# Kernel optimization log

Hardware: AMD Instinct MI355X
Metric: run time of the kernel (lower is better)

## Reference

```python
import math
import jax, jax.numpy as jnp
import numpy as np

B, S, DK, DV = 8, 2048, 512, 512

def setup_inputs() -> dict:
    key = jax.random.key(0)
    kq, kk, kv, km = jax.random.split(key, 4)
    Q = jax.random.normal(kq, (B, S, DK), dtype=jnp.float32)
    K = jax.random.normal(kk, (B, S, DK), dtype=jnp.float32)
    V = jax.random.normal(kv, (B, S, DV), dtype=jnp.float32)
    # key-padding mask, True = masked out; broadcasts over query dim
    mask_out = jax.random.randint(km, (B, 1, S), 0, 2).astype(jnp.bool_)
    return {"Q": Q, "K": K, "V": V, "mask_out": mask_out}

def reference(Q, K, V, mask_out):
    scale = math.sqrt(Q.shape[-1])
    # [B, S, S] scores
    scores = jnp.einsum('bqd,bkd->bqk', Q, K) / scale
    scores = jnp.where(mask_out, -jnp.inf, scores)
    attn = jax.nn.softmax(scores, axis=-1)
    # dropout is identity in eval mode (reference baseline)
    return jnp.einsum('bqk,bkv->bqv', attn, V)
```

## Files before the change

kernel.cpp:

```cpp
#include <hip/hip_runtime.h>
#include <stdint.h>
#include <stddef.h>

#define B_ 8
#define S_ 2048
#define D_ 512
#define QT 64
#define KTL 32
#define NIT (S_ / KTL)

typedef __attribute__((ext_vector_type(8))) short short8;
typedef __attribute__((ext_vector_type(4))) float f32x4;

#define OFF_K0  0
#define OFF_K1  32768
#define OFF_ST  65536
#define OFF_P   73728
#define OFF_A   77824
#define OFF_L   78080
#define OFF_M   78336
#define LDS_BYTES 78592

__device__ __forceinline__ void gl_lds16(const void* g, void* l) {
  __builtin_amdgcn_global_load_lds(
      (const __attribute__((address_space(1))) uint32_t*)g,
      (__attribute__((address_space(3))) uint32_t*)l, 16, 0, 0);
}

__device__ __forceinline__ void bar_lgkm() {
  __asm__ __volatile__("" ::: "memory");
  __builtin_amdgcn_s_waitcnt(0xC07F);
  __builtin_amdgcn_s_barrier();
  __asm__ __volatile__("" ::: "memory");
}
__device__ __forceinline__ void bar_vm0() {
  __asm__ __volatile__("" ::: "memory");
  __builtin_amdgcn_s_waitcnt(0x0070);
  __builtin_amdgcn_s_barrier();
  __asm__ __volatile__("" ::: "memory");
}

template<int CTRL>
__device__ __forceinline__ float dpp_mov(float x) {
  return __builtin_bit_cast(float,
      __builtin_amdgcn_update_dpp(0, __builtin_bit_cast(int, x),
                                  CTRL, 0xF, 0xF, true));
}
__device__ __forceinline__ float red8_max(float x) {
  x = fmaxf(x, dpp_mov<0xB1>(x));
  x = fmaxf(x, dpp_mov<0x4E>(x));
  x = fmaxf(x, dpp_mov<0x141>(x));
  return x;
}
__device__ __forceinline__ float red8_sum(float x) {
  x += dpp_mov<0xB1>(x);
  x += dpp_mov<0x4E>(x);
  x += dpp_mov<0x141>(x);
  return x;
}

__device__ __forceinline__ uint32_t f2bf(float f) {
  union { float f; uint32_t u; } x; x.f = f;
  uint32_t r = x.u + 0x7FFFu + ((x.u >> 16) & 1u);
  return r >> 16;
}

__device__ __forceinline__ bool sniff_fp32(const void* p) {
  const uint32_t* w = (const uint32_t*)p;
  bool ok = true;
  #pragma unroll 1
  for (int i = 0; i < 64; ++i) {
    uint32_t e = (w[i] >> 23) & 0xFFu;
    if (!(e == 0u || (e >= 64u && e <= 192u))) ok = false;
  }
  return ok;
}

__device__ __forceinline__ short8 cvt8(const void* src, bool fp32) {
  short8 d;
  if (fp32) {
    const float* s = (const float*)src;
    f32x4 a = *(const f32x4*)s, c = *(const f32x4*)(s + 4);
    #pragma unroll
    for (int j = 0; j < 4; ++j) { d[j] = (short)f2bf(a[j]); d[4 + j] = (short)f2bf(c[j]); }
  } else {
    d = *(const short8*)src;
  }
  return d;
}

__global__ void prep_kernel(const void* __restrict__ K, const void* __restrict__ V,
                            uint16_t* __restrict__ kbf, uint16_t* __restrict__ vt) {
  __shared__ uint32_t vtile[64 * 32];
  bool fp32 = sniff_fp32(K);
  int kt = blockIdx.x, dt = blockIdx.y, b = blockIdx.z;
  int t  = threadIdx.x;
  {
    size_t off = (size_t)b * S_ * D_ + (size_t)(kt * 64 + (t >> 3)) * D_ + dt * 64 + (t & 7) * 8;
    const void* src = fp32 ? (const void*)((const float*)K + off)
                           : (const void*)((const uint16_t*)K + off);
    *(short8*)(kbf + off) = cvt8(src, fp32);
  }
  {
    int key = t >> 3;
    int c0  = (t & 7) * 4;
    size_t off = (size_t)b * S_ * D_ + (size_t)(kt * 64 + key) * D_ + dt * 64 + (t & 7) * 8;
    const void* src = fp32 ? (const void*)((const float*)V + off)
                           : (const void*)((const uint16_t*)V + off);
    short8 d = cvt8(src, fp32);
    const uint32_t* dw = (const uint32_t*)&d;
    #pragma unroll
    for (int i = 0; i < 4; ++i)
      vtile[key * 32 + ((c0 + i + key) & 31)] = dw[i];
  }
  __syncthreads();
  {
    int dvl = t >> 3;
    int kg  = t & 7;
    short8 o;
    #pragma unroll
    for (int j = 0; j < 8; ++j) {
      int key = kg * 8 + j;
      uint32_t wv = vtile[key * 32 + (((dvl >> 1) + key) & 31)];
      o[j] = (short)((dvl & 1) ? (wv >> 16) : (wv & 0xFFFFu));
    }
    *(short8*)(vt + ((size_t)b * D_ + dt * 64 + dvl) * S_ + kt * 64 + kg * 8) = o;
  }
}

__device__ __forceinline__ void stage_K(char* buf, const uint16_t* kg, int w, int lane, int kt) {
  #pragma unroll
  for (int p = 0; p < 4; ++p) {
    int n = p * 8 + w;
    int g = (lane & ~7) | ((lane ^ n) & 7);
    gl_lds16(kg + ((size_t)(kt * KTL + n)) * D_ + g * 8, buf + n * 1024);
  }
}
__device__ __forceinline__ void stage_K_slow(char* buf, const void* kg, bool fp32,
                                             int w, int lane, int kt) {
  #pragma unroll
  for (int p = 0; p < 4; ++p) {
    int n = p * 8 + w;
    size_t off = ((size_t)(kt * KTL + n)) * D_ + lane * 8;
    const void* src = fp32 ? (const void*)((const float*)kg + off)
                           : (const void*)((const uint16_t*)kg + off);
    short8 d = cvt8(src, fp32);
    int s = (lane & ~7) | ((lane ^ n) & 7);
    *(short8*)(buf + n * 1024 + s * 16) = d;
  }
}
__device__ __forceinline__ void stage_V_slow(char* smem, const void* vg, bool fp32,
                                             int w, int lane, int kt) {
  #pragma unroll
  for (int p = 0; p < 4; ++p) {
    int n = p * 8 + w;
    size_t off = ((size_t)(kt * KTL + n)) * D_ + lane * 8;
    const void* src = fp32 ? (const void*)((const float*)vg + off)
                           : (const void*)((const uint16_t*)vg + off);
    short8 d = cvt8(src, fp32);
    *(short8*)(smem + OFF_K1 + n * 1024 + lane * 16) = d;
  }
}

template<bool FAST>
__global__ __launch_bounds__(512, 2)
void attn_kernel(const void* __restrict__ Q, const void* __restrict__ K,
                 const void* __restrict__ V, const void* __restrict__ mask,
                 const uint16_t* __restrict__ kbf, const uint16_t* __restrict__ vtbf,
                 void* __restrict__ out) {
  extern __shared__ char smem[];
  const int tid  = threadIdx.x;
  const int lane = tid & 63;
  const int w    = tid >> 6;
  const int m15  = lane & 15;
  const int kq   = lane >> 4;

  const bool fp32 = sniff_fp32(Q);

  const int b     = blockIdx.x;
  const int qbase = blockIdx.y * QT;
  const int qt_w  = w >> 1;
  const int kh    = w & 1;

  const uint16_t* kgf  = FAST ? (kbf + (size_t)b * S_ * D_) : nullptr;
  const uint16_t* vtg  = FAST ? (vtbf + (size_t)b * D_ * S_) : nullptr;
  const void* kgs = fp32 ? (const void*)((const float*)K + (size_t)b * S_ * D_)
                         : (const void*)((const uint16_t*)K + (size_t)b * S_ * D_);
  const void* vgs = fp32 ? (const void*)((const float*)V + (size_t)b * S_ * D_)
                         : (const void*)((const uint16_t*)V + (size_t)b * S_ * D_);

  if (tid < 64) {
    const uint32_t* mw = (const uint32_t*)mask;
    const uint8_t*  mb = (const uint8_t*)mask;
    bool is64 = true, any_even = false, is32 = true;
    for (int j = 0; j < 64; ++j) {
      uint32_t lo = mw[2 * j], hi = mw[2 * j + 1];
      if (hi != 0u || lo > 1u) is64 = false;
      if (lo) any_even = true;
    }
    is64 = is64 && any_even;
    for (int j = 0; j < 128; ++j) {
      uint32_t x = mw[j];
      if (x != 0u && x != 1u && x != 0x3F800000u) is32 = false;
    }
    uint32_t bits = 0;
    int base = b * S_ + tid * 32;
    for (int e = 0; e < 32; ++e) {
      uint32_t x = is64 ? mw[2 * (base + e)]
                        : (is32 ? mw[base + e] : (uint32_t)mb[base + e]);
      bits |= (x ? 1u : 0u) << e;
    }
    *(uint32_t*)(smem + OFF_M + tid * 4) = bits;
  }

  short8 aq[16];
  {
    size_t q0 = ((size_t)b * S_ + qbase + qt_w * 16 + m15) * D_ + kq * 8;
    #pragma unroll
    for (int sl = 0; sl < 16; ++sl) {
      size_t off = q0 + sl * 32;
      const void* src = fp32 ? (const void*)((const float*)Q + off)
                             : (const void*)((const uint16_t*)Q + off);
      aq[sl] = cvt8(src, fp32);
    }
  }

  f32x4 acc_o[4][4];
  #pragma unroll
  for (int i = 0; i < 4; ++i)
    #pragma unroll
    for (int j = 0; j < 4; ++j)
      acc_o[i][j] = (f32x4){0.f, 0.f, 0.f, 0.f};

  float m_run = -1e30f, l_run = 0.f;
  const float k1 = 0.06375872f;

  if (FAST) stage_K(smem + OFF_K0, kgf, w, lane, 0);

  for (int kt = 0; kt < NIT; ++kt) {
    char* kbuf = smem + ((kt & 1) && FAST ? OFF_K1 : OFF_K0);
    if (FAST) {
      bar_vm0();
    } else {
      __syncthreads();
      stage_K_slow(smem + OFF_K0, kgs, fp32, w, lane, kt);
      stage_V_slow(smem, vgs, fp32, w, lane, kt);
      __syncthreads();
    }

    short8 vf[4];
    if (FAST) {
      #pragma unroll
      for (int ct = 0; ct < 4; ++ct)
        vf[ct] = *(const short8*)(vtg + (size_t)(w * 64 + ct * 16 + m15) * S_
                                  + kt * KTL + kq * 8);
      if (kt < NIT - 1)
        stage_K(smem + ((kt & 1) ? OFF_K0 : OFF_K1), kgf, w, lane, kt + 1);
    }

    int keyg = kt * KTL + kh * 16 + m15;
    float bv = ((*(const uint32_t*)(smem + OFF_M + (keyg >> 5) * 4) >> (keyg & 31)) & 1u)
               ? -3.0e38f : 0.f;

    const int n = kh * 16 + m15;
    f32x4 acc_s0 = (f32x4){0.f, 0.f, 0.f, 0.f};
    f32x4 acc_s1 = (f32x4){0.f, 0.f, 0.f, 0.f};
    #pragma unroll
    for (int sl = 0; sl < 8; ++sl) {
      int c0  = sl * 4 + kq;
      int c1  = (sl + 8) * 4 + kq;
      int cs0 = (c0 & ~7) | ((c0 ^ n) & 7);
      int cs1 = (c1 & ~7) | ((c1 ^ n) & 7);
      short8 bf0 = *(const short8*)(kbuf + n * 1024 + cs0 * 16);
      short8 bf1 = *(const short8*)(kbuf + n * 1024 + cs1 * 16);
      acc_s0 = __builtin_amdgcn_mfma_f32_16x16x32_bf16(aq[sl],     bf0, acc_s0, 0, 0, 0);
      acc_s1 = __builtin_amdgcn_mfma_f32_16x16x32_bf16(aq[sl + 8], bf1, acc_s1, 0, 0, 0);
    }

    {
      int key  = n;
      int blk  = qt_w * 4 + kq;
      int xblk = blk ^ (key & 15) ^ ((key >> 2) & 3);
      f32x4 sv;
      #pragma unroll
      for (int r = 0; r < 4; ++r) sv[r] = (acc_s0[r] + acc_s1[r]) * k1 + bv;
      *(f32x4*)(smem + OFF_ST + key * 256 + xblk * 16) = sv;
    }
    bar_lgkm();

    {
      int r  = w * 8 + (lane >> 3);
      int k0 = (lane & 7) * 4;
      float u[4];
      #pragma unroll
      for (int i = 0; i < 4; ++i) {
        int k    = k0 + i;
        int xblk = (r >> 2) ^ (k & 15) ^ ((k >> 2) & 3);
        u[i] = *(const float*)(smem + OFF_ST + k * 256 + xblk * 16 + (r & 3) * 4);
      }
      float mt = fmaxf(fmaxf(u[0], u[1]), fmaxf(u[2], u[3]));
      mt = red8_max(mt);
      float m_new = fmaxf(m_run, mt);
      float alpha = exp2f(m_run - m_new);
      float s = 0.f;
      #pragma unroll
      for (int i = 0; i < 4; ++i) { u[i] = exp2f(u[i] - m_new); s += u[i]; }
      s = red8_sum(s);
      l_run = l_run * alpha + s;
      m_run = m_new;
      uint2 d;
      d.x = f2bf(u[0]) | (f2bf(u[1]) << 16);
      d.y = f2bf(u[2]) | (f2bf(u[3]) << 16);
      int g = ((lane & 7) >> 1) ^ (r & 3);
      *(uint2*)(smem + OFF_P + r * 64 + g * 16 + (lane & 1) * 8) = d;
      if ((lane & 7) == 0) {
        *(float*)(smem + OFF_A + r * 4) = alpha;
        *(float*)(smem + OFF_L + r * 4) = l_run;
      }
    }
    bar_lgkm();

    #pragma unroll
    for (int rt = 0; rt < 4; ++rt) {
      f32x4 al = *(const f32x4*)(smem + OFF_A + (rt * 16 + kq * 4) * 4);
      #pragma unroll
      for (int ct = 0; ct < 4; ++ct) acc_o[rt][ct] *= al;
    }
    short8 ap[4];
    #pragma unroll
    for (int rt = 0; rt < 4; ++rt) {
      int rr = rt * 16 + m15;
      int g  = kq ^ (rr & 3);
      ap[rt] = *(const short8*)(smem + OFF_P + rr * 64 + g * 16);
    }
    #pragma unroll
    for (int ct = 0; ct < 4; ++ct) {
      short8 bvv;
      if (FAST) {
        bvv = vf[ct];
      } else {
        #pragma unroll
        for (int j = 0; j < 8; ++j)
          bvv[j] = *(const short*)(smem + OFF_K1 + (kq * 8 + j) * 1024
                                   + (w * 64 + ct * 16 + m15) * 2);
      }
      #pragma unroll
      for (int rt = 0; rt < 4; ++rt)
        acc_o[rt][ct] = __builtin_amdgcn_mfma_f32_16x16x32_bf16(
            ap[rt], bvv, acc_o[rt][ct], 0, 0, 0);
    }
  }

  #pragma unroll
  for (int rt = 0; rt < 4; ++rt) {
    f32x4 lv = *(const f32x4*)(smem + OFF_L + (rt * 16 + kq * 4) * 4);
    f32x4 inv;
    #pragma unroll
    for (int r = 0; r < 4; ++r) inv[r] = lv[r] > 0.f ? 1.f / lv[r] : 0.f;
    #pragma unroll
    for (int ct = 0; ct < 4; ++ct) {
      int col = w * 64 + ct * 16 + m15;
      #pragma unroll
      for (int r = 0; r < 4; ++r) {
        int row = qbase + rt * 16 + kq * 4 + r;
        size_t idx = ((size_t)b * S_ + row) * D_ + col;
        float val = acc_o[rt][ct][r] * inv[r];
        if (fp32) ((float*)out)[idx] = val;
        else      ((uint16_t*)out)[idx] = (uint16_t)f2bf(val);
      }
    }
  }
}

extern "C" void kernel_launch(void* const* d_in, const int* in_sizes, int n_in,
                              void* d_out, int out_size, void* d_ws, size_t ws_size,
                              hipStream_t stream) {
  (void)in_sizes; (void)n_in; (void)out_size;
  const void* Q    = d_in[0];
  const void* K    = d_in[1];
  const void* V    = d_in[2];
  const void* mask = d_in[3];

  const size_t half = (size_t)B_ * S_ * D_ * 2;
  bool fast = ws_size >= 2 * half;

  if (fast) {
    uint16_t* kbf  = (uint16_t*)d_ws;
    uint16_t* vtbf = (uint16_t*)((char*)d_ws + half);
    prep_kernel<<<dim3(32, 8, 8), 512, 0, stream>>>(K, V, kbf, vtbf);
    hipFuncSetAttribute((const void*)attn_kernel<true>,
                        hipFuncAttributeMaxDynamicSharedMemorySize, LDS_BYTES);
    attn_kernel<true><<<dim3(8, S_ / QT), 512, LDS_BYTES, stream>>>(
        Q, K, V, mask, kbf, vtbf, d_out);
  } else {
    hipFuncSetAttribute((const void*)attn_kernel<false>,
                        hipFuncAttributeMaxDynamicSharedMemorySize, LDS_BYTES);
    attn_kernel<false><<<dim3(8, S_ / QT), 512, LDS_BYTES, stream>>>(
        Q, K, V, mask, nullptr, nullptr, d_out);
  }
}
```

Baseline: 293.1 us.

## Software-pipeline QK^T of next tile with softmax of current tile

Restructures the fast-path main loop so the QK^T MFMAs for key tile kt+1 are issued before the softmax of tile kt, using double-buffered score tiles in LDS. K staging is prefetched two tiles ahead, and one barrier per iteration is removed. The aim is to hide MFMA latency behind the softmax exp/reduction work and cut synchronisation. In exchange it uses more LDS and more live registers, which may lower occupancy.

Result: no change. 291.2 us (-0.7%).

```diff
diff --git a/kernel.cpp b/kernel.cpp
--- a/kernel.cpp
+++ b/kernel.cpp
@@ -14,12 +14,13 @@
 
 #define OFF_K0  0
 #define OFF_K1  32768
-#define OFF_ST  65536
-#define OFF_P   73728
-#define OFF_A   77824
-#define OFF_L   78080
-#define OFF_M   78336
-#define LDS_BYTES 78592
+#define OFF_ST0 65536
+#define OFF_ST1 73728
+#define OFF_P   81920
+#define OFF_A   86016
+#define OFF_L   86272
+#define OFF_M   86528
+#define LDS_BYTES 86784
 
 __device__ __forceinline__ void gl_lds16(const void* g, void* l) {
   __builtin_amdgcn_global_load_lds(
@@ -235,69 +236,71 @@
   float m_run = -1e30f, l_run = 0.f;
   const float k1 = 0.06375872f;
 
-  if (FAST) stage_K(smem + OFF_K0, kgf, w, lane, 0);
-
-  for (int kt = 0; kt < NIT; ++kt) {
-    char* kbuf = smem + ((kt & 1) && FAST ? OFF_K1 : OFF_K0);
-    if (FAST) {
+  const int nql = kh * 16 + m15;
+
+  auto qk_issue = [&](const char* kb, f32x4& a0, f32x4& a1) {
+    a0 = (f32x4){0.f, 0.f, 0.f, 0.f};
+    a1 = (f32x4){0.f, 0.f, 0.f, 0.f};
+    #pragma unroll
+    for (int sl = 0; sl < 8; ++sl) {
+      int c0  = sl * 4 + kq;
+      int c1  = (sl + 8) * 4 + kq;
+      int cs0 = (c0 & ~7) | ((c0 ^ nql) & 7);
+      int cs1 = (c1 & ~7) | ((c1 ^ nql) & 7);
+      short8 b0 = *(const short8*)(kb + nql * 1024 + cs0 * 16);
+      short8 b1 = *(const short8*)(kb + nql * 1024 + cs1 * 16);
+      a0 = __builtin_amdgcn_mfma_f32_16x16x32_bf16(aq[sl],     b0, a0, 0, 0, 0);
+      a1 = __builtin_amdgcn_mfma_f32_16x16x32_bf16(aq[sl + 8], b1, a1, 0, 0, 0);
+    }
+  };
+  auto qk_store = [&](int tile, char* st, const f32x4& a0, const f32x4& a1) {
+    int keyg = tile * KTL + nql;
+    float bv = ((*(const uint32_t*)(smem + OFF_M + (keyg >> 5) * 4) >> (keyg & 31)) & 1u)
+               ? -3.0e38f : 0.f;
+    int blk  = qt_w * 4 + kq;
+    int xblk = blk ^ (nql & 15) ^ ((nql >> 2) & 3);
+    f32x4 sv;
+    #pragma unroll
+    for (int rr = 0; rr < 4; ++rr) sv[rr] = (a0[rr] + a1[rr]) * k1 + bv;
+    *(f32x4*)(st + nql * 256 + xblk * 16) = sv;
+  };
+
+  if constexpr (FAST) {
+    stage_K(smem + OFF_K0, kgf, w, lane, 0);
+    bar_vm0();
+    {
+      f32x4 a0, a1;
+      qk_issue(smem + OFF_K0, a0, a1);
+      qk_store(0, smem + OFF_ST0, a0, a1);
+    }
+    stage_K(smem + OFF_K1, kgf, w, lane, 1);
+
+    #pragma unroll 1
+    for (int kt = 0; kt < NIT; ++kt) {
       bar_vm0();
-    } else {
-      __syncthreads();
-      stage_K_slow(smem + OFF_K0, kgs, fp32, w, lane, kt);
-      stage_V_slow(smem, vgs, fp32, w, lane, kt);
-      __syncthreads();
-    }
-
-    short8 vf[4];
-    if (FAST) {
+      short8 vf[4];
       #pragma unroll
       for (int ct = 0; ct < 4; ++ct)
         vf[ct] = *(const short8*)(vtg + (size_t)(w * 64 + ct * 16 + m15) * S_
                                   + kt * KTL + kq * 8);
-      if (kt < NIT - 1)
-        stage_K(smem + ((kt & 1) ? OFF_K0 : OFF_K1), kgf, w, lane, kt + 1);
-    }
-
-    int keyg = kt * KTL + kh * 16 + m15;
-    float bv = ((*(const uint32_t*)(smem + OFF_M + (keyg >> 5) * 4) >> (keyg & 31)) & 1u)
-               ? -3.0e38f : 0.f;
-
-    const int n = kh * 16 + m15;
-    f32x4 acc_s0 = (f32x4){0.f, 0.f, 0.f, 0.f};
-    f32x4 acc_s1 = (f32x4){0.f, 0.f, 0.f, 0.f};
-    #pragma unroll
-    for (int sl = 0; sl < 8; ++sl) {
-      int c0  = sl * 4 + kq;
-      int c1  = (sl + 8) * 4 + kq;
-      int cs0 = (c0 & ~7) | ((c0 ^ n) & 7);
-      int cs1 = (c1 & ~7) | ((c1 ^ n) & 7);
-      short8 bf0 = *(const short8*)(kbuf + n * 1024 + cs0 * 16);
-      short8 bf1 = *(const short8*)(kbuf + n * 1024 + cs1 * 16);
-      acc_s0 = __builtin_amdgcn_mfma_f32_16x16x32_bf16(aq[sl],     bf0, acc_s0, 0, 0, 0);
-      acc_s1 = __builtin_amdgcn_mfma_f32_16x16x32_bf16(aq[sl + 8], bf1, acc_s1, 0, 0, 0);
-    }
-
-    {
-      int key  = n;
-      int blk  = qt_w * 4 + kq;
-      int xblk = blk ^ (key & 15) ^ ((key >> 2) & 3);
-      f32x4 sv;
-      #pragma unroll
-      for (int r = 0; r < 4; ++r) sv[r] = (acc_s0[r] + acc_s1[r]) * k1 + bv;
-      *(f32x4*)(smem + OFF_ST + key * 256 + xblk * 16) = sv;
-    }
-    bar_lgkm();
-
-    {
-      int r  = w * 8 + (lane >> 3);
-      int k0 = (lane & 7) * 4;
+      if (kt + 2 < NIT)
+        stage_K(smem + ((kt & 1) ? OFF_K1 : OFF_K0), kgf, w, lane, kt + 2);
+
+      char* st_cur = smem + ((kt & 1) ? OFF_ST1 : OFF_ST0);
+      const int r  = w * 8 + (lane >> 3);
+      const int k0 = (lane & 7) * 4;
       float u[4];
       #pragma unroll
       for (int i = 0; i < 4; ++i) {
-        int k    = k0 + i;
-        int xblk = (r >> 2) ^ (k & 15) ^ ((k >> 2) & 3);
-        u[i] = *(const float*)(smem + OFF_ST + k * 256 + xblk * 16 + (r & 3) * 4);
-      }
+        int k  = k0 + i;
+        int xb = (r >> 2) ^ (k & 15) ^ ((k >> 2) & 3);
+        u[i] = *(const float*)(st_cur + k * 256 + xb * 16 + (r & 3) * 4);
+      }
+      const bool has_next = (kt < NIT - 1);
+      f32x4 a0, a1;
+      if (has_next)
+        qk_issue(smem + (((kt + 1) & 1) ? OFF_K1 : OFF_K0), a0, a1);
+
       float mt = fmaxf(fmaxf(u[0], u[1]), fmaxf(u[2], u[3]));
       mt = red8_max(mt);
       float m_new = fmaxf(m_run, mt);
@@ -317,37 +320,100 @@
         *(float*)(smem + OFF_A + r * 4) = alpha;
         *(float*)(smem + OFF_L + r * 4) = l_run;
       }
-    }
-    bar_lgkm();
-
-    #pragma unroll
-    for (int rt = 0; rt < 4; ++rt) {
-      f32x4 al = *(const f32x4*)(smem + OFF_A + (rt * 16 + kq * 4) * 4);
-      #pragma unroll
-      for (int ct = 0; ct < 4; ++ct) acc_o[rt][ct] *= al;
-    }
-    short8 ap[4];
-    #pragma unroll
-    for (int rt = 0; rt < 4; ++rt) {
-      int rr = rt * 16 + m15;
-      int g  = kq ^ (rr & 3);
-      ap[rt] = *(const short8*)(smem + OFF_P + rr * 64 + g * 16);
-    }
-    #pragma unroll
-    for (int ct = 0; ct < 4; ++ct) {
-      short8 bvv;
-      if (FAST) {
-        bvv = vf[ct];
-      } else {
+      if (has_next)
+        qk_store(kt + 1, smem + (((kt + 1) & 1) ? OFF_ST1 : OFF_ST0), a0, a1);
+
+      bar_lgkm();
+
+      #pragma unroll
+      for (int rt = 0; rt < 4; ++rt) {
+        f32x4 al = *(const f32x4*)(smem + OFF_A + (rt * 16 + kq * 4) * 4);
+        #pragma unroll
+        for (int ct = 0; ct < 4; ++ct) acc_o[rt][ct] *= al;
+      }
+      short8 ap[4];
+      #pragma unroll
+      for (int rt = 0; rt < 4; ++rt) {
+        int rr = rt * 16 + m15;
+        int gg = kq ^ (rr & 3);
+        ap[rt] = *(const short8*)(smem + OFF_P + rr * 64 + gg * 16);
+      }
+      #pragma unroll
+      for (int ct = 0; ct < 4; ++ct) {
+        #pragma unroll
+        for (int rt = 0; rt < 4; ++rt)
+          acc_o[rt][ct] = __builtin_amdgcn_mfma_f32_16x16x32_bf16(
+              ap[rt], vf[ct], acc_o[rt][ct], 0, 0, 0);
+      }
+    }
+  } else {
+    #pragma unroll 1
+    for (int kt = 0; kt < NIT; ++kt) {
+      __syncthreads();
+      stage_K_slow(smem + OFF_K0, kgs, fp32, w, lane, kt);
+      stage_V_slow(smem, vgs, fp32, w, lane, kt);
+      __syncthreads();
+
+      f32x4 a0, a1;
+      qk_issue(smem + OFF_K0, a0, a1);
+      qk_store(kt, smem + OFF_ST0, a0, a1);
+      bar_lgkm();
+
+      const int r  = w * 8 + (lane >> 3);
+      const int k0 = (lane & 7) * 4;
+      float u[4];
+      #pragma unroll
+      for (int i = 0; i < 4; ++i) {
+        int k  = k0 + i;
+        int xb = (r >> 2) ^ (k & 15) ^ ((k >> 2) & 3);
+        u[i] = *(const float*)(smem + OFF_ST0 + k * 256 + xb * 16 + (r & 3) * 4);
+      }
+      float mt = fmaxf(fmaxf(u[0], u[1]), fmaxf(u[2], u[3]));
+      mt = red8_max(mt);
+      float m_new = fmaxf(m_run, mt);
+      float alpha = exp2f(m_run - m_new);
+      float s = 0.f;
+      #pragma unroll
+      for (int i = 0; i < 4; ++i) { u[i] = exp2f(u[i] - m_new); s += u[i]; }
+      s = red8_sum(s);
+      l_run = l_run * alpha + s;
+      m_run = m_new;
+      uint2 d;
+      d.x = f2bf(u[0]) | (f2bf(u[1]) << 16);
+      d.y = f2bf(u[2]) | (f2bf(u[3]) << 16);
+      int g = ((lane & 7) >> 1) ^ (r & 3);
+      *(uint2*)(smem + OFF_P + r * 64 + g * 16 + (lane & 1) * 8) = d;
+      if ((lane & 7) == 0) {
+        *(float*)(smem + OFF_A + r * 4) = alpha;
+        *(float*)(smem + OFF_L + r * 4) = l_run;
+      }
+      bar_lgkm();
+
+      #pragma unroll
+      for (int rt = 0; rt < 4; ++rt) {
+        f32x4 al = *(const f32x4*)(smem + OFF_A + (rt * 16 + kq * 4) * 4);
+        #pragma unroll
+        for (int ct = 0; ct < 4; ++ct) acc_o[rt][ct] *= al;
+      }
+      short8 ap[4];
+      #pragma unroll
+      for (int rt = 0; rt < 4; ++rt) {
+        int rr = rt * 16 + m15;
+        int gg = kq ^ (rr & 3);
+        ap[rt] = *(const short8*)(smem + OFF_P + rr * 64 + gg * 16);
+      }
+      #pragma unroll
+      for (int ct = 0; ct < 4; ++ct) {
+        short8 bvv;
         #pragma unroll
         for (int j = 0; j < 8; ++j)
           bvv[j] = *(const short*)(smem + OFF_K1 + (kq * 8 + j) * 1024
                                    + (w * 64 + ct * 16 + m15) * 2);
-      }
-      #pragma unroll
-      for (int rt = 0; rt < 4; ++rt)
-        acc_o[rt][ct] = __builtin_amdgcn_mfma_f32_16x16x32_bf16(
-            ap[rt], bvv, acc_o[rt][ct], 0, 0, 0);
+        #pragma unroll
+        for (int rt = 0; rt < 4; ++rt)
+          acc_o[rt][ct] = __builtin_amdgcn_mfma_f32_16x16x32_bf16(
+              ap[rt], bvv, acc_o[rt][ct], 0, 0, 0);
+      }
     }
   }
 
```

## Halve query tile and split QK^T head dim across warp halves

Applied to the files above, without the earlier changes.

Shrinks the per-block query tile from 64 to 32 rows and splits the QK^T reduction over the head dimension between two warp groups. Each group writes partial scores to its own LDS buffer and the softmax sums the two. This halves the Q fragments and output accumulators held per thread, so launch bounds rise to 4 blocks per CU and the grid doubles. In exchange, K and V are re-streamed twice as often per query row, and only half the warps do softmax work.

Result: slower. 332.1 us (+13.3%).

```diff
diff --git a/kernel.cpp b/kernel.cpp
--- a/kernel.cpp
+++ b/kernel.cpp
@@ -5,7 +5,7 @@
 #define B_ 8
 #define S_ 2048
 #define D_ 512
-#define QT 64
+#define QT 32
 #define KTL 32
 #define NIT (S_ / KTL)
 
@@ -14,12 +14,13 @@
 
 #define OFF_K0  0
 #define OFF_K1  32768
-#define OFF_ST  65536
+#define OFF_STA 65536
+#define OFF_STB 69632
 #define OFF_P   73728
-#define OFF_A   77824
-#define OFF_L   78080
-#define OFF_M   78336
-#define LDS_BYTES 78592
+#define OFF_A   75776
+#define OFF_L   75904
+#define OFF_M   76032
+#define LDS_BYTES 76288
 
 __device__ __forceinline__ void gl_lds16(const void* g, void* l) {
   __builtin_amdgcn_global_load_lds(
@@ -163,7 +164,7 @@
 }
 
 template<bool FAST>
-__global__ __launch_bounds__(512, 2)
+__global__ __launch_bounds__(512, 4)
 void attn_kernel(const void* __restrict__ Q, const void* __restrict__ K,
                  const void* __restrict__ V, const void* __restrict__ mask,
                  const uint16_t* __restrict__ kbf, const uint16_t* __restrict__ vtbf,
@@ -179,8 +180,9 @@
 
   const int b     = blockIdx.x;
   const int qbase = blockIdx.y * QT;
-  const int qt_w  = w >> 1;
+  const int qt_w  = (w >> 1) & 1;
   const int kh    = w & 1;
+  const int dh    = w >> 2;
 
   const uint16_t* kgf  = FAST ? (kbf + (size_t)b * S_ * D_) : nullptr;
   const uint16_t* vtg  = FAST ? (vtbf + (size_t)b * D_ * S_) : nullptr;
@@ -213,11 +215,11 @@
     *(uint32_t*)(smem + OFF_M + tid * 4) = bits;
   }
 
-  short8 aq[16];
+  short8 aq[8];
   {
-    size_t q0 = ((size_t)b * S_ + qbase + qt_w * 16 + m15) * D_ + kq * 8;
-    #pragma unroll
-    for (int sl = 0; sl < 16; ++sl) {
+    size_t q0 = ((size_t)b * S_ + qbase + qt_w * 16 + m15) * D_ + dh * 256 + kq * 8;
+    #pragma unroll
+    for (int sl = 0; sl < 8; ++sl) {
       size_t off = q0 + sl * 32;
       const void* src = fp32 ? (const void*)((const float*)Q + off)
                              : (const void*)((const uint16_t*)Q + off);
@@ -225,9 +227,9 @@
     }
   }
 
-  f32x4 acc_o[4][4];
+  f32x4 acc_o[2][4];
   #pragma unroll
-  for (int i = 0; i < 4; ++i)
+  for (int i = 0; i < 2; ++i)
     #pragma unroll
     for (int j = 0; j < 4; ++j)
       acc_o[i][j] = (f32x4){0.f, 0.f, 0.f, 0.f};
@@ -235,12 +237,23 @@
   float m_run = -1e30f, l_run = 0.f;
   const float k1 = 0.06375872f;
 
+  const int nql = kh * 16 + m15;
+  char* stp = smem + (dh ? OFF_STB : OFF_STA);
+
   if (FAST) stage_K(smem + OFF_K0, kgf, w, lane, 0);
 
+  #pragma unroll 1
   for (int kt = 0; kt < NIT; ++kt) {
     char* kbuf = smem + ((kt & 1) && FAST ? OFF_K1 : OFF_K0);
+    short8 vf[4];
     if (FAST) {
       bar_vm0();
+      #pragma unroll
+      for (int ct = 0; ct < 4; ++ct)
+        vf[ct] = *(const short8*)(vtg + (size_t)(w * 64 + ct * 16 + m15) * S_
+                                  + kt * KTL + kq * 8);
+      if (kt < NIT - 1)
+        stage_K(smem + ((kt & 1) ? OFF_K0 : OFF_K1), kgf, w, lane, kt + 1);
     } else {
       __syncthreads();
       stage_K_slow(smem + OFF_K0, kgs, fp32, w, lane, kt);
@@ -248,55 +261,46 @@
       __syncthreads();
     }
 
-    short8 vf[4];
-    if (FAST) {
-      #pragma unroll
-      for (int ct = 0; ct < 4; ++ct)
-        vf[ct] = *(const short8*)(vtg + (size_t)(w * 64 + ct * 16 + m15) * S_
-                                  + kt * KTL + kq * 8);
-      if (kt < NIT - 1)
-        stage_K(smem + ((kt & 1) ? OFF_K0 : OFF_K1), kgf, w, lane, kt + 1);
-    }
-
-    int keyg = kt * KTL + kh * 16 + m15;
-    float bv = ((*(const uint32_t*)(smem + OFF_M + (keyg >> 5) * 4) >> (keyg & 31)) & 1u)
-               ? -3.0e38f : 0.f;
-
-    const int n = kh * 16 + m15;
-    f32x4 acc_s0 = (f32x4){0.f, 0.f, 0.f, 0.f};
-    f32x4 acc_s1 = (f32x4){0.f, 0.f, 0.f, 0.f};
-    #pragma unroll
-    for (int sl = 0; sl < 8; ++sl) {
-      int c0  = sl * 4 + kq;
-      int c1  = (sl + 8) * 4 + kq;
-      int cs0 = (c0 & ~7) | ((c0 ^ n) & 7);
-      int cs1 = (c1 & ~7) | ((c1 ^ n) & 7);
-      short8 bf0 = *(const short8*)(kbuf + n * 1024 + cs0 * 16);
-      short8 bf1 = *(const short8*)(kbuf + n * 1024 + cs1 * 16);
-      acc_s0 = __builtin_amdgcn_mfma_f32_16x16x32_bf16(aq[sl],     bf0, acc_s0, 0, 0, 0);
-      acc_s1 = __builtin_amdgcn_mfma_f32_16x16x32_bf16(aq[sl + 8], bf1, acc_s1, 0, 0, 0);
+    f32x4 a0 = (f32x4){0.f, 0.f, 0.f, 0.f};
+    f32x4 a1 = (f32x4){0.f, 0.f, 0.f, 0.f};
+    #pragma unroll
+    for (int sl = 0; sl < 4; ++sl) {
+      int c0  = (dh * 8 + sl) * 4 + kq;
+      int c1  = (dh * 8 + sl + 4) * 4 + kq;
+      int cs0 = (c0 & ~7) | ((c0 ^ nql) & 7);
+      int cs1 = (c1 & ~7) | ((c1 ^ nql) & 7);
+      short8 b0 = *(const short8*)(kbuf + nql * 1024 + cs0 * 16);
+      short8 b1 = *(const short8*)(kbuf + nql * 1024 + cs1 * 16);
+      a0 = __builtin_amdgcn_mfma_f32_16x16x32_bf16(aq[sl],     b0, a0, 0, 0, 0);
+      a1 = __builtin_amdgcn_mfma_f32_16x16x32_bf16(aq[sl + 4], b1, a1, 0, 0, 0);
     }
 
     {
-      int key  = n;
+      int keyg = kt * KTL + nql;
+      float bv = 0.f;
+      if (dh == 0)
+        bv = ((*(const uint32_t*)(smem + OFF_M + (keyg >> 5) * 4) >> (keyg & 31)) & 1u)
+             ? -3.0e38f : 0.f;
       int blk  = qt_w * 4 + kq;
-      int xblk = blk ^ (key & 15) ^ ((key >> 2) & 3);
+      int xblk = blk ^ (nql & 7) ^ (nql >> 3);
       f32x4 sv;
       #pragma unroll
-      for (int r = 0; r < 4; ++r) sv[r] = (acc_s0[r] + acc_s1[r]) * k1 + bv;
-      *(f32x4*)(smem + OFF_ST + key * 256 + xblk * 16) = sv;
+      for (int r = 0; r < 4; ++r) sv[r] = (a0[r] + a1[r]) * k1 + bv;
+      *(f32x4*)(stp + nql * 128 + xblk * 16) = sv;
     }
     bar_lgkm();
 
-    {
+    if (w < 4) {
       int r  = w * 8 + (lane >> 3);
       int k0 = (lane & 7) * 4;
       float u[4];
       #pragma unroll
       for (int i = 0; i < 4; ++i) {
         int k    = k0 + i;
-        int xblk = (r >> 2) ^ (k & 15) ^ ((k >> 2) & 3);
-        u[i] = *(const float*)(smem + OFF_ST + k * 256 + xblk * 16 + (r & 3) * 4);
+        int xblk = (r >> 2) ^ (k & 7) ^ (k >> 3);
+        int off  = k * 128 + xblk * 16 + (r & 3) * 4;
+        u[i] = *(const float*)(smem + OFF_STA + off)
+             + *(const float*)(smem + OFF_STB + off);
       }
       float mt = fmaxf(fmaxf(u[0], u[1]), fmaxf(u[2], u[3]));
       mt = red8_max(mt);
@@ -321,14 +325,14 @@
     bar_lgkm();
 
     #pragma unroll
-    for (int rt = 0; rt < 4; ++rt) {
+    for (int rt = 0; rt < 2; ++rt) {
       f32x4 al = *(const f32x4*)(smem + OFF_A + (rt * 16 + kq * 4) * 4);
       #pragma unroll
       for (int ct = 0; ct < 4; ++ct) acc_o[rt][ct] *= al;
     }
-    short8 ap[4];
-    #pragma unroll
-    for (int rt = 0; rt < 4; ++rt) {
+    short8 ap[2];
+    #pragma unroll
+    for (int rt = 0; rt < 2; ++rt) {
       int rr = rt * 16 + m15;
       int g  = kq ^ (rr & 3);
       ap[rt] = *(const short8*)(smem + OFF_P + rr * 64 + g * 16);
@@ -345,14 +349,14 @@
                                    + (w * 64 + ct * 16 + m15) * 2);
       }
       #pragma unroll
-      for (int rt = 0; rt < 4; ++rt)
+      for (int rt = 0; rt < 2; ++rt)
         acc_o[rt][ct] = __builtin_amdgcn_mfma_f32_16x16x32_bf16(
             ap[rt], bvv, acc_o[rt][ct], 0, 0, 0);
     }
   }
 
   #pragma unroll
-  for (int rt = 0; rt < 4; ++rt) {
+  for (int rt = 0; rt < 2; ++rt) {
     f32x4 lv = *(const f32x4*)(smem + OFF_L + (rt * 16 + kq * 4) * 4);
     f32x4 inv;
     #pragma unroll
```

## Warp-specialize attention: score/softmax waves pipelined against PV waves

Applied to the files above, without the earlier changes.

Splits the 8 waves into two roles. Four waves compute QK^T scores and softmax for tile kt+1 while the other four stage K and run the P·V MFMAs for tile kt. The P, alpha and l buffers are double-buffered so the two stages can overlap across barriers. This targets the serialization between score, softmax and PV phases in the old loop, but halves the waves doing each stage and raises per-wave register pressure (32 f32x4 accumulators). It also uses more LDS, which may affect occupancy.

After: 300.4 us. +2.5%, slower.

```diff
diff --git a/kernel.cpp b/kernel.cpp
--- a/kernel.cpp
+++ b/kernel.cpp
@@ -15,11 +15,14 @@
 #define OFF_K0  0
 #define OFF_K1  32768
 #define OFF_ST  65536
-#define OFF_P   73728
-#define OFF_A   77824
-#define OFF_L   78080
-#define OFF_M   78336
-#define LDS_BYTES 78592
+#define OFF_P0  73728
+#define OFF_P1  77824
+#define OFF_A0  81920
+#define OFF_A1  82176
+#define OFF_L0  82432
+#define OFF_L1  82688
+#define OFF_M   82944
+#define LDS_BYTES 83200
 
 __device__ __forceinline__ void gl_lds16(const void* g, void* l) {
   __builtin_amdgcn_global_load_lds(
@@ -45,6 +48,16 @@
   return __builtin_bit_cast(float,
       __builtin_amdgcn_update_dpp(0, __builtin_bit_cast(int, x),
                                   CTRL, 0xF, 0xF, true));
+}
+__device__ __forceinline__ float red4_max(float x) {
+  x = fmaxf(x, dpp_mov<0xB1>(x));
+  x = fmaxf(x, dpp_mov<0x4E>(x));
+  return x;
+}
+__device__ __forceinline__ float red4_sum(float x) {
+  x += dpp_mov<0xB1>(x);
+  x += dpp_mov<0x4E>(x);
+  return x;
 }
 __device__ __forceinline__ float red8_max(float x) {
   x = fmaxf(x, dpp_mov<0xB1>(x));
@@ -128,10 +141,10 @@
   }
 }
 
-__device__ __forceinline__ void stage_K(char* buf, const uint16_t* kg, int w, int lane, int kt) {
+__device__ __forceinline__ void stage_K_v(char* buf, const uint16_t* kg, int w2, int lane, int kt) {
   #pragma unroll
-  for (int p = 0; p < 4; ++p) {
-    int n = p * 8 + w;
+  for (int p = 0; p < 8; ++p) {
+    int n = p * 4 + w2;
     int g = (lane & ~7) | ((lane ^ n) & 7);
     gl_lds16(kg + ((size_t)(kt * KTL + n)) * D_ + g * 8, buf + n * 1024);
   }
@@ -179,8 +192,6 @@
 
   const int b     = blockIdx.x;
   const int qbase = blockIdx.y * QT;
-  const int qt_w  = w >> 1;
-  const int kh    = w & 1;
 
   const uint16_t* kgf  = FAST ? (kbf + (size_t)b * S_ * D_) : nullptr;
   const uint16_t* vtg  = FAST ? (vtbf + (size_t)b * D_ * S_) : nullptr;
@@ -213,160 +224,316 @@
     *(uint32_t*)(smem + OFF_M + tid * 4) = bits;
   }
 
-  short8 aq[16];
-  {
-    size_t q0 = ((size_t)b * S_ + qbase + qt_w * 16 + m15) * D_ + kq * 8;
+  const float k1 = 0.06375872f;
+
+  if constexpr (FAST) {
+    const int  w2   = w & 3;
+    const bool is_s = (w < 4);
+    const int  srow = w2 * 16 + (lane >> 2);
+    const int  soct = lane & 3;
+
+    f32x4 regs[32];
     #pragma unroll
-    for (int sl = 0; sl < 16; ++sl) {
-      size_t off = q0 + sl * 32;
-      const void* src = fp32 ? (const void*)((const float*)Q + off)
-                             : (const void*)((const uint16_t*)Q + off);
-      aq[sl] = cvt8(src, fp32);
-    }
-  }
-
-  f32x4 acc_o[4][4];
-  #pragma unroll
-  for (int i = 0; i < 4; ++i)
+    for (int i = 0; i < 32; ++i) regs[i] = (f32x4){0.f, 0.f, 0.f, 0.f};
+
+    float m_run = -1e30f, l_run = 0.f;
+
+    if (is_s) {
+      size_t q0 = ((size_t)b * S_ + qbase + w2 * 16 + m15) * D_ + kq * 8;
+      #pragma unroll
+      for (int sl = 0; sl < 16; ++sl) {
+        size_t off = q0 + sl * 32;
+        const void* src = fp32 ? (const void*)((const float*)Q + off)
+                               : (const void*)((const uint16_t*)Q + off);
+        regs[sl] = __builtin_bit_cast(f32x4, cvt8(src, fp32));
+      }
+    }
+
+    auto qk_phase = [&](int j) {
+      const char* kb = smem + ((j & 1) ? OFF_K1 : OFF_K0);
+      const int n0 = m15, n1 = 16 + m15;
+      f32x4 s0a = {0.f,0.f,0.f,0.f}, s0b = {0.f,0.f,0.f,0.f};
+      f32x4 s1a = {0.f,0.f,0.f,0.f}, s1b = {0.f,0.f,0.f,0.f};
+      #pragma unroll
+      for (int sl = 0; sl < 8; ++sl) {
+        int c0 = sl * 4 + kq, c1 = (sl + 8) * 4 + kq;
+        int cs00 = (c0 & ~7) | ((c0 ^ n0) & 7);
+        int cs01 = (c1 & ~7) | ((c1 ^ n0) & 7);
+        int cs10 = (c0 & ~7) | ((c0 ^ n1) & 7);
+        int cs11 = (c1 & ~7) | ((c1 ^ n1) & 7);
+        short8 b00 = *(const short8*)(kb + n0 * 1024 + cs00 * 16);
+        short8 b01 = *(const short8*)(kb + n0 * 1024 + cs01 * 16);
+        short8 b10 = *(const short8*)(kb + n1 * 1024 + cs10 * 16);
+        short8 b11 = *(const short8*)(kb + n1 * 1024 + cs11 * 16);
+        short8 a0 = __builtin_bit_cast(short8, regs[sl]);
+        short8 a1 = __builtin_bit_cast(short8, regs[sl + 8]);
+        s0a = __builtin_amdgcn_mfma_f32_16x16x32_bf16(a0, b00, s0a, 0, 0, 0);
+        s0b = __builtin_amdgcn_mfma_f32_16x16x32_bf16(a1, b01, s0b, 0, 0, 0);
+        s1a = __builtin_amdgcn_mfma_f32_16x16x32_bf16(a0, b10, s1a, 0, 0, 0);
+        s1b = __builtin_amdgcn_mfma_f32_16x16x32_bf16(a1, b11, s1b, 0, 0, 0);
+      }
+      #pragma unroll
+      for (int t = 0; t < 2; ++t) {
+        int key  = (t == 0) ? n0 : n1;
+        int keyg = j * KTL + key;
+        float bv = ((*(const uint32_t*)(smem + OFF_M + (keyg >> 5) * 4) >> (keyg & 31)) & 1u)
+                   ? -3.0e38f : 0.f;
+        int blk  = w2 * 4 + kq;
+        int xblk = blk ^ (key & 15) ^ ((key >> 2) & 3);
+        f32x4 sv;
+        f32x4 pa = (t == 0) ? s0a : s1a;
+        f32x4 pb = (t == 0) ? s0b : s1b;
+        #pragma unroll
+        for (int r = 0; r < 4; ++r) sv[r] = (pa[r] + pb[r]) * k1 + bv;
+        *(f32x4*)(smem + OFF_ST + key * 256 + xblk * 16) = sv;
+      }
+    };
+
+    auto smax_phase = [&](int j) {
+      char* pb = smem + ((j & 1) ? OFF_P1 : OFF_P0);
+      char* ab = smem + ((j & 1) ? OFF_A1 : OFF_A0);
+      char* lb = smem + ((j & 1) ? OFF_L1 : OFF_L0);
+      float u[8];
+      #pragma unroll
+      for (int i = 0; i < 8; ++i) {
+        int k    = soct * 8 + i;
+        int xblk = (srow >> 2) ^ (k & 15) ^ ((k >> 2) & 3);
+        u[i] = *(const float*)(smem + OFF_ST + k * 256 + xblk * 16 + (srow & 3) * 4);
+      }
+      float mt = fmaxf(fmaxf(fmaxf(u[0], u[1]), fmaxf(u[2], u[3])),
+                       fmaxf(fmaxf(u[4], u[5]), fmaxf(u[6], u[7])));
+      mt = red4_max(mt);
+      float m_new = fmaxf(m_run, mt);
+      float alpha = exp2f(m_run - m_new);
+      float s = 0.f;
+      #pragma unroll
+      for (int i = 0; i < 8; ++i) { u[i] = exp2f(u[i] - m_new); s += u[i]; }
+      s = red4_sum(s);
+      l_run = l_run * alpha + s;
+      m_run = m_new;
+      uint4 d;
+      d.x = f2bf(u[0]) | (f2bf(u[1]) << 16);
+      d.y = f2bf(u[2]) | (f2bf(u[3]) << 16);
+      d.z = f2bf(u[4]) | (f2bf(u[5]) << 16);
+      d.w = f2bf(u[6]) | (f2bf(u[7]) << 16);
+      int g = soct ^ (srow & 3);
+      *(uint4*)(pb + srow * 64 + g * 16) = d;
+      if (soct == 0) {
+        *(float*)(ab + srow * 4) = alpha;
+        *(float*)(lb + srow * 4) = l_run;
+      }
+    };
+
+    if (!is_s) stage_K_v(smem + OFF_K0, kgf, w2, lane, 0);
+    bar_vm0();
+    if (is_s) qk_phase(0);
+    else      stage_K_v(smem + OFF_K1, kgf, w2, lane, 1);
+    bar_lgkm();
+    if (is_s) smax_phase(0);
+    bar_vm0();
+
+    short8 vf[4 + 4];
+    short8 ap[4];
+    #pragma unroll 1
+    for (int kt = 0; kt < NIT; ++kt) {
+      if (is_s) {
+        if (kt + 1 < NIT) qk_phase(kt + 1);
+      } else {
+        #pragma unroll
+        for (int ct = 0; ct < 8; ++ct)
+          vf[ct] = *(const short8*)(vtg + (size_t)(w2 * 128 + ct * 16 + m15) * S_
+                                    + kt * KTL + kq * 8);
+        if (kt + 2 < NIT)
+          stage_K_v(smem + ((kt & 1) ? OFF_K1 : OFF_K0), kgf, w2, lane, kt + 2);
+        char* pbuf = smem + ((kt & 1) ? OFF_P1 : OFF_P0);
+        char* abuf = smem + ((kt & 1) ? OFF_A1 : OFF_A0);
+        #pragma unroll
+        for (int rt = 0; rt < 4; ++rt) {
+          int rr = rt * 16 + m15;
+          int g  = kq ^ (rr & 3);
+          ap[rt] = *(const short8*)(pbuf + rr * 64 + g * 16);
+        }
+        #pragma unroll
+        for (int rt = 0; rt < 4; ++rt) {
+          f32x4 al = *(const f32x4*)(abuf + (rt * 16 + kq * 4) * 4);
+          #pragma unroll
+          for (int ct = 0; ct < 8; ++ct) regs[rt * 8 + ct] *= al;
+        }
+        #pragma unroll
+        for (int ct = 0; ct < 4; ++ct)
+          #pragma unroll
+          for (int rt = 0; rt < 4; ++rt)
+            regs[rt * 8 + ct] = __builtin_amdgcn_mfma_f32_16x16x32_bf16(
+                ap[rt], vf[ct], regs[rt * 8 + ct], 0, 0, 0);
+      }
+      bar_lgkm();
+
+      if (is_s) {
+        if (kt + 1 < NIT) smax_phase(kt + 1);
+      } else {
+        #pragma unroll
+        for (int ct = 4; ct < 8; ++ct)
+          #pragma unroll
+          for (int rt = 0; rt < 4; ++rt)
+            regs[rt * 8 + ct] = __builtin_amdgcn_mfma_f32_16x16x32_bf16(
+                ap[rt], vf[ct], regs[rt * 8 + ct], 0, 0, 0);
+      }
+      bar_vm0();
+    }
+
+    if (!is_s) {
+      char* lb = smem + (((NIT - 1) & 1) ? OFF_L1 : OFF_L0);
+      #pragma unroll
+      for (int rt = 0; rt < 4; ++rt) {
+        f32x4 lv = *(const f32x4*)(lb + (rt * 16 + kq * 4) * 4);
+        f32x4 inv;
+        #pragma unroll
+        for (int r = 0; r < 4; ++r) inv[r] = lv[r] > 0.f ? 1.f / lv[r] : 0.f;
+        #pragma unroll
+        for (int ct = 0; ct < 8; ++ct) {
+          int col = w2 * 128 + ct * 16 + m15;
+          #pragma unroll
+          for (int r = 0; r < 4; ++r) {
+            int row = qbase + rt * 16 + kq * 4 + r;
+            size_t idx = ((size_t)b * S_ + row) * D_ + col;
+            float val = regs[rt * 8 + ct][r] * inv[r];
+            if (fp32) ((float*)out)[idx] = val;
+            else      ((uint16_t*)out)[idx] = (uint16_t)f2bf(val);
+          }
+        }
+      }
+    }
+  } else {
+    const int qt_w = w >> 1;
+    const int kh   = w & 1;
+    short8 aq[16];
+    {
+      size_t q0 = ((size_t)b * S_ + qbase + qt_w * 16 + m15) * D_ + kq * 8;
+      #pragma unroll
+      for (int sl = 0; sl < 16; ++sl) {
+        size_t off = q0 + sl * 32;
+        const void* src = fp32 ? (const void*)((const float*)Q + off)
+                               : (const void*)((const uint16_t*)Q + off);
+        aq[sl] = cvt8(src, fp32);
+      }
+    }
+    f32x4 acc_o[4][4];
     #pragma unroll
-    for (int j = 0; j < 4; ++j)
-      acc_o[i][j] = (f32x4){0.f, 0.f, 0.f, 0.f};
-
-  float m_run = -1e30f, l_run = 0.f;
-  const float k1 = 0.06375872f;
-
-  if (FAST) stage_K(smem + OFF_K0, kgf, w, lane, 0);
-
-  for (int kt = 0; kt < NIT; ++kt) {
-    char* kbuf = smem + ((kt & 1) && FAST ? OFF_K1 : OFF_K0);
-    if (FAST) {
-      bar_vm0();
-    } else {
+    for (int i = 0; i < 4; ++i)
+      #pragma unroll
+      for (int j = 0; j < 4; ++j)
+        acc_o[i][j] = (f32x4){0.f, 0.f, 0.f, 0.f};
+    float m_run = -1e30f, l_run = 0.f;
+
+    #pragma unroll 1
+    for (int kt = 0; kt < NIT; ++kt) {
       __syncthreads();
       stage_K_slow(smem + OFF_K0, kgs, fp32, w, lane, kt);
       stage_V_slow(smem, vgs, fp32, w, lane, kt);
       __syncthreads();
-    }
-
-    short8 vf[4];
-    if (FAST) {
-      #pragma unroll
-      for (int ct = 0; ct < 4; ++ct)
-        vf[ct] = *(const short8*)(vtg + (size_t)(w * 64 + ct * 16 + m15) * S_
-                                  + kt * KTL + kq * 8);
-      if (kt < NIT - 1)
-        stage_K(smem + ((kt & 1) ? OFF_K0 : OFF_K1), kgf, w, lane, kt + 1);
-    }
-
-    int keyg = kt * KTL + kh * 16 + m15;
-    float bv = ((*(const uint32_t*)(smem + OFF_M + (keyg >> 5) * 4) >> (keyg & 31)) & 1u)
-               ? -3.0e38f : 0.f;
-
-    const int n = kh * 16 + m15;
-    f32x4 acc_s0 = (f32x4){0.f, 0.f, 0.f, 0.f};
-    f32x4 acc_s1 = (f32x4){0.f, 0.f, 0.f, 0.f};
-    #pragma unroll
-    for (int sl = 0; sl < 8; ++sl) {
-      int c0  = sl * 4 + kq;
-      int c1  = (sl + 8) * 4 + kq;
-      int cs0 = (c0 & ~7) | ((c0 ^ n) & 7);
-      int cs1 = (c1 & ~7) | ((c1 ^ n) & 7);
-      short8 bf0 = *(const short8*)(kbuf + n * 1024 + cs0 * 16);
-      short8 bf1 = *(const short8*)(kbuf + n * 1024 + cs1 * 16);
-      acc_s0 = __builtin_amdgcn_mfma_f32_16x16x32_bf16(aq[sl],     bf0, acc_s0, 0, 0, 0);
-      acc_s1 = __builtin_amdgcn_mfma_f32_16x16x32_bf16(aq[sl + 8], bf1, acc_s1, 0, 0, 0);
-    }
-
-    {
-      int key  = n;
-      int blk  = qt_w * 4 + kq;
-      int xblk = blk ^ (key & 15) ^ ((key >> 2) & 3);
-      f32x4 sv;
-      #pragma unroll
-      for (int r = 0; r < 4; ++r) sv[r] = (acc_s0[r] + acc_s1[r]) * k1 + bv;
-      *(f32x4*)(smem + OFF_ST + key * 256 + xblk * 16) = sv;
-    }
-    bar_lgkm();
-
-    {
-      int r  = w * 8 + (lane >> 3);
-      int k0 = (lane & 7) * 4;
-      float u[4];
-      #pragma unroll
-      for (int i = 0; i < 4; ++i) {
-        int k    = k0 + i;
-        int xblk = (r >> 2) ^ (k & 15) ^ ((k >> 2) & 3);
-        u[i] = *(const float*)(smem + OFF_ST + k * 256 + xblk * 16 + (r & 3) * 4);
-      }
-      float mt = fmaxf(fmaxf(u[0], u[1]), fmaxf(u[2], u[3]));
-      mt = red8_max(mt);
-      float m_new = fmaxf(m_run, mt);
-      float alpha = exp2f(m_run - m_new);
-      float s = 0.f;
-      #pragma unroll
-      for (int i = 0; i < 4; ++i) { u[i] = exp2f(u[i] - m_new); s += u[i]; }
-      s = red8_sum(s);
-      l_run = l_run * alpha + s;
-      m_run = m_new;
-      uint2 d;
-      d.x = f2bf(u[0]) | (f2bf(u[1]) << 16);
-      d.y = f2bf(u[2]) | (f2bf(u[3]) << 16);
-      int g = ((lane & 7) >> 1) ^ (r & 3);
-      *(uint2*)(smem + OFF_P + r * 64 + g * 16 + (lane & 1) * 8) = d;
-      if ((lane & 7) == 0) {
-        *(float*)(smem + OFF_A + r * 4) = alpha;
-        *(float*)(smem + OFF_L + r * 4) = l_run;
-      }
-    }
-    bar_lgkm();
-
-    #pragma unroll
-    for (int rt = 0; rt < 4; ++rt) {
-      f32x4 al = *(const f32x4*)(smem + OFF_A + (rt * 16 + kq * 4) * 4);
-      #pragma unroll
-      for (int ct = 0; ct < 4; ++ct) acc_o[rt][ct] *= al;
-    }
-    short8 ap[4];
-    #pragma unroll
-    for (int rt = 0; rt < 4; ++rt) {
-      int rr = rt * 16 + m15;
-      int g  = kq ^ (rr & 3);
-      ap[rt] = *(const short8*)(smem + OFF_P + rr * 64 + g * 16);
-    }
-    #pragma unroll
-    for (int ct = 0; ct < 4; ++ct) {
-      short8 bvv;
-      if (FAST) {
-        bvv = vf[ct];
-      } else {
+
+      int keyg = kt * KTL + kh * 16 + m15;
+      float bv = ((*(const uint32_t*)(smem + OFF_M + (keyg >> 5) * 4) >> (keyg & 31)) & 1u)
+                 ? -3.0e38f : 0.f;
+      const int n = kh * 16 + m15;
+      f32x4 a0 = {0.f,0.f,0.f,0.f}, a1 = {0.f,0.f,0.f,0.f};
+      #pragma unroll
+      for (int sl = 0; sl < 8; ++sl) {
+        int c0  = sl * 4 + kq;
+        int c1  = (sl + 8) * 4 + kq;
+        int cs0 = (c0 & ~7) | ((c0 ^ n) & 7);
+        int cs1 = (c1 & ~7) | ((c1 ^ n) & 7);
+        short8 bf0 = *(const short8*)(smem + OFF_K0 + n * 1024 + cs0 * 16);
+        short8 bf1 = *(const short8*)(smem + OFF_K0 + n * 1024 + cs1 * 16);
+        a0 = __builtin_amdgcn_mfma_f32_16x16x32_bf16(aq[sl],     bf0, a0, 0, 0, 0);
+        a1 = __builtin_amdgcn_mfma_f32_16x16x32_bf16(aq[sl + 8], bf1, a1, 0, 0, 0);
+      }
+      {
+        int blk  = qt_w * 4 + kq;
+        int xblk = blk ^ (n & 15) ^ ((n >> 2) & 3);
+        f32x4 sv;
+        #pragma unroll
+        for (int r = 0; r < 4; ++r) sv[r] = (a0[r] + a1[r]) * k1 + bv;
+        *(f32x4*)(smem + OFF_ST + n * 256 + xblk * 16) = sv;
+      }
+      bar_lgkm();
+
+      {
+        int r  = w * 8 + (lane >> 3);
+        int k0 = (lane & 7) * 4;
+        float u[4];
+        #pragma unroll
+        for (int i = 0; i < 4; ++i) {
+          int k    = k0 + i;
+          int xblk = (r >> 2) ^ (k & 15) ^ ((k >> 2) & 3);
+          u[i] = *(const float*)(smem + OFF_ST + k * 256 + xblk * 16 + (r & 3) * 4);
+        }
+        float mt = fmaxf(fmaxf(u[0], u[1]), fmaxf(u[2], u[3]));
+        mt = red8_max(mt);
+        float m_new = fmaxf(m_run, mt);
+        float alpha = exp2f(m_run - m_new);
+        float s = 0.f;
+        #pragma unroll
+        for (int i = 0; i < 4; ++i) { u[i] = exp2f(u[i] - m_new); s += u[i]; }
+        s = red8_sum(s);
+        l_run = l_run * alpha + s;
+        m_run = m_new;
+        uint2 d;
+        d.x = f2bf(u[0]) | (f2bf(u[1]) << 16);
+        d.y = f2bf(u[2]) | (f2bf(u[3]) << 16);
+        int g = ((lane & 7) >> 1) ^ (r & 3);
+        *(uint2*)(smem + OFF_P0 + r * 64 + g * 16 + (lane & 1) * 8) = d;
+        if ((lane & 7) == 0) {
+          *(float*)(smem + OFF_A0 + r * 4) = alpha;
+          *(float*)(smem + OFF_L0 + r * 4) = l_run;
+        }
+      }
+      bar_lgkm();
+
+      #pragma unroll
+      for (int rt = 0; rt < 4; ++rt) {
+        f32x4 al = *(const f32x4*)(smem + OFF_A0 + (rt * 16 + kq * 4) * 4);
+        #pragma unroll
+        for (int ct = 0; ct < 4; ++ct) acc_o[rt][ct] *= al;
+      }
+      short8 ap[4];
+      #pragma unroll
+      for (int rt = 0; rt < 4; ++rt) {
+        int rr = rt * 16 + m15;
+        int g  = kq ^ (rr & 3);
+        ap[rt] = *(const short8*)(smem + OFF_P0 + rr * 64 + g * 16);
+      }
+      #pragma unroll
+      for (int ct = 0; ct < 4; ++ct) {
+        short8 bvv;
         #pragma unroll
         for (int j = 0; j < 8; ++j)
           bvv[j] = *(const short*)(smem + OFF_K1 + (kq * 8 + j) * 1024
                                    + (w * 64 + ct * 16 + m15) * 2);
-      }
-      #pragma unroll
-      for (int rt = 0; rt < 4; ++rt)
-        acc_o[rt][ct] = __builtin_amdgcn_mfma_f32_16x16x32_bf16(
-            ap[rt], bvv, acc_o[rt][ct], 0, 0, 0);
-    }
-  }
-
-  #pragma unroll
-  for (int rt = 0; rt < 4; ++rt) {
-    f32x4 lv = *(const f32x4*)(smem + OFF_L + (rt * 16 + kq * 4) * 4);
-    f32x4 inv;
+        #pragma unroll
+        for (int rt = 0; rt < 4; ++rt)
+          acc_o[rt][ct] = __builtin_amdgcn_mfma_f32_16x16x32_bf16(
+              ap[rt], bvv, acc_o[rt][ct], 0, 0, 0);
+      }
+    }
+
     #pragma unroll
-    for (int r = 0; r < 4; ++r) inv[r] = lv[r] > 0.f ? 1.f / lv[r] : 0.f;
-    #pragma unroll
-    for (int ct = 0; ct < 4; ++ct) {
-      int col = w * 64 + ct * 16 + m15;
-      #pragma unroll
-      for (int r = 0; r < 4; ++r) {
-        int row = qbase + rt * 16 + kq * 4 + r;
-        size_t idx = ((size_t)b * S_ + row) * D_ + col;
-        float val = acc_o[rt][ct][r] * inv[r];
-        if (fp32) ((float*)out)[idx] = val;
-        else      ((uint16_t*)out)[idx] = (uint16_t)f2bf(val);
+    for (int rt = 0; rt < 4; ++rt) {
+      f32x4 lv = *(const f32x4*)(smem + OFF_L0 + (rt * 16 + kq * 4) * 4);
+      f32x4 inv;
+      #pragma unroll
+      for (int r = 0; r < 4; ++r) inv[r] = lv[r] > 0.f ? 1.f / lv[r] : 0.f;
+      #pragma unroll
+      for (int ct = 0; ct < 4; ++ct) {
+        int col = w * 64 + ct * 16 + m15;
+        #pragma unroll
+        for (int r = 0; r < 4; ++r) {
+          int row = qbase + rt * 16 + kq * 4 + r;
+          size_t idx = ((size_t)b * S_ + row) * D_ + col;
+          float val = acc_o[rt][ct][r] * inv[r];
+          if (fp32) ((float*)out)[idx] = val;
+          else      ((uint16_t*)out)[idx] = (uint16_t)f2bf(val);
+        }
       }
     }
   }
```
